# Performance work log

Hardware: AMD Instinct MI355X
Metric: run time of the kernel (lower is better)

The kernel has to match this reference:

```python
import jax, jax.numpy as jnp
import numpy as np

E, T, D_IN, D_H = 8, 2048, 2048, 5632


def setup_inputs() -> dict:
    key = jax.random.key(0)
    kx, kg, kd, ku = jax.random.split(key, 4)
    scale = 0.02  # init_std-like scaling for weights
    return {
        "x": jax.random.normal(kx, (E, T, D_IN), dtype=jnp.float32),
        "gate_proj": jax.random.normal(kg, (E, D_IN, D_H), dtype=jnp.float32) * scale,
        "down_proj": jax.random.normal(kd, (E, D_IN, D_H), dtype=jnp.float32) * scale,
        "up_proj": jax.random.normal(ku, (E, D_H, D_IN), dtype=jnp.float32) * scale,
        "tokens_per_expert": T,
    }


def reference(x, gate_proj, down_proj, up_proj, tokens_per_expert):
    # ep_size=1: dispatch/combine are identity. Grouped SwiGLU per expert.
    # x: [E, T, d_in]; gate/down: [E, d_in, d_h]; up: [E, d_h, d_in]
    g = jnp.einsum('etd,edh->eth', x, gate_proj)
    u = jnp.einsum('etd,edh->eth', x, down_proj)
    h = jax.nn.silu(g) * u  # [E, T, d_h]
    out = jnp.einsum('eth,ehd->etd', h, up_proj)  # [E, T, d_in]
    return out
```

## Files before the change

kernel.cpp:

```cpp
#include <hip/hip_runtime.h>
#include <hip/hip_bf16.h>


#define NEXP 8
#define TT   2048
#define DIN  2048
#define DH   5632
#define KP   2080

using short8 = __attribute__((ext_vector_type(8))) short;
using f32x4  = __attribute__((ext_vector_type(4))) float;

static __device__ __forceinline__ unsigned short f2bf(float f) {
    unsigned int i = __float_as_uint(f);
    return (unsigned short)((i + 0x7FFFu + ((i >> 16) & 1u)) >> 16);
}
static __device__ __forceinline__ void gld16(const void* g, void* l) {
    __builtin_amdgcn_global_load_lds(
        (const __attribute__((address_space(1))) void*)g,
        (__attribute__((address_space(3))) void*)l, 16, 0, 0);
}

__global__ __launch_bounds__(512, 2) void gemm_gu(
    const unsigned short* __restrict__ Xb,
    const unsigned short* __restrict__ Wgt,
    const unsigned short* __restrict__ Wdt,
    unsigned short* __restrict__ Hb)
{
    __shared__ __align__(16) unsigned short lds[81920];

    const int tid  = threadIdx.x;
    const int wave = tid >> 6, lane = tid & 63;
    const int l15 = lane & 15, l4 = lane >> 4;
    const int wr = wave >> 2, wc = wave & 3;

    const int bid = blockIdx.x;
    const int e   = bid & 7;
    const int cu  = bid >> 3;
    const int m0  = (cu & 7) * 256;
    const int nb  = cu >> 3;

    const unsigned short* Ae = Xb + (size_t)e * TT * KP;
    unsigned short* He = Hb + (size_t)e * TT * DH;

    const int c0 = tid, c1 = 512 + tid;
    const int cs0 = c0 ^ ((c0 >> 3) & 7), cs1 = c1 ^ ((c1 >> 3) & 7);
    const int row0 = cs0 >> 3, col0 = (cs0 & 7) * 8;
    const int row1 = cs1 >> 3, col1 = (cs1 & 7) * 8;

    int ibA[4][2], ibB[2][2];
#pragma unroll
    for (int s = 0; s < 4; ++s)
#pragma unroll
        for (int ks = 0; ks < 2; ++ks) {
            const int r = wr * 64 + s * 16 + l15;
            ibA[s][ks] = (r * 128 + ks * 64 + l4 * 16) ^ ((r & 7) << 4);
        }
#pragma unroll
    for (int s = 0; s < 2; ++s)
#pragma unroll
        for (int ks = 0; ks < 2; ++ks) {
            const int r = wc * 32 + s * 16 + l15;
            ibB[s][ks] = (r * 128 + ks * 64 + l4 * 16) ^ ((r & 7) << 4);
        }

    f32x4 acc[8][4] = {};
    short8 Aq[4][2], Gq[2][2], Dq[2][2];

    char* ldsb = (char*)lds;
    auto stageA = [&](int ro, int kk, int so) {
        gld16(Ae + (size_t)(m0 + ro + row0) * KP + (kk + col0), ldsb + so + wave * 1024);
        gld16(Ae + (size_t)(m0 + ro + row1) * KP + (kk + col1), ldsb + so + 8192 + wave * 1024);
    };
    auto stageW = [&](const unsigned short* p, int kk, int so) {
        gld16(p + (size_t)row0 * KP + (kk + col0), ldsb + so + wave * 1024);
        gld16(p + (size_t)row1 * KP + (kk + col1), ldsb + so + 8192 + wave * 1024);
    };
    auto w10 = [](int x) { return x >= 10 ? x - 10 : x; };

    const size_t NSTEP = (size_t)512 * KP;
    const unsigned short* Gc = Wgt + (size_t)e * DH * KP + (size_t)(nb * 128) * KP;
    const unsigned short* Dc = Wdt + (size_t)e * DH * KP + (size_t)(nb * 128) * KP;

    stageA(0, 0, 0 << 14);  stageW(Gc, 0, 1 << 14);  stageW(Dc, 0, 2 << 14);  stageA(128, 0, 3 << 14);
    stageA(0, 64, 4 << 14); stageW(Gc, 64, 5 << 14); stageW(Dc, 64, 6 << 14);
    asm volatile("s_waitcnt vmcnt(6)" ::: "memory");
    asm volatile("s_barrier" ::: "memory");

    const char* ldsc = (const char*)lds;
    int q = 0;
    for (int i = 0; i < 11; ++i) {
        const unsigned short* Gn = Gc + NSTEP;
        const unsigned short* Dn = Dc + NSTEP;
        for (int t = 0; t < 32; ++t) {
            const int g = (i << 5) + t;
            const int sA0 = q << 14;
            const int sG  = w10(q + 1) << 14;
            const int sD  = w10(q + 2) << 14;
            const int sA1 = w10(q + 3) << 14;
            const int stA1 = w10(q + 7) << 14;
            const int stA0 = w10(q + 8) << 14;
            const int stG  = w10(q + 9) << 14;
            const int stD  = sA0;

#pragma unroll
            for (int s = 0; s < 4; ++s) {
                Aq[s][0] = *(const short8*)(ldsc + sA0 + ibA[s][0]);
                Aq[s][1] = *(const short8*)(ldsc + sA0 + ibA[s][1]);
            }
#pragma unroll
            for (int s = 0; s < 2; ++s) {
                Gq[s][0] = *(const short8*)(ldsc + sG + ibB[s][0]);
                Gq[s][1] = *(const short8*)(ldsc + sG + ibB[s][1]);
                Dq[s][0] = *(const short8*)(ldsc + sD + ibB[s][0]);
                Dq[s][1] = *(const short8*)(ldsc + sD + ibB[s][1]);
            }
            if (i < 10 || t + 1 < 32)
                stageA(128, ((t + 1) & 31) * 64, stA1);
            asm volatile("s_waitcnt lgkmcnt(0)" ::: "memory");
            __builtin_amdgcn_sched_barrier(0);
            __builtin_amdgcn_s_setprio(1);
#pragma unroll
            for (int m = 0; m < 4; ++m)
#pragma unroll
                for (int n = 0; n < 2; ++n) {
                    acc[m][n] = __builtin_amdgcn_mfma_f32_16x16x32_bf16(Aq[m][0], Gq[n][0], acc[m][n], 0, 0, 0);
                    acc[m][n] = __builtin_amdgcn_mfma_f32_16x16x32_bf16(Aq[m][1], Gq[n][1], acc[m][n], 0, 0, 0);
                }
            __builtin_amdgcn_s_setprio(0);
            if (i < 10 || t + 2 < 32)
                stageA(0, ((t + 2) & 31) * 64, stA0);
            __builtin_amdgcn_s_setprio(1);
#pragma unroll
            for (int m = 0; m < 4; ++m)
#pragma unroll
                for (int n = 0; n < 2; ++n) {
                    acc[m][2 + n] = __builtin_amdgcn_mfma_f32_16x16x32_bf16(Aq[m][0], Dq[n][0], acc[m][2 + n], 0, 0, 0);
                    acc[m][2 + n] = __builtin_amdgcn_mfma_f32_16x16x32_bf16(Aq[m][1], Dq[n][1], acc[m][2 + n], 0, 0, 0);
                }
            __builtin_amdgcn_s_setprio(0);
#pragma unroll
            for (int s = 0; s < 4; ++s) {
                Aq[s][0] = *(const short8*)(ldsc + sA1 + ibA[s][0]);
                Aq[s][1] = *(const short8*)(ldsc + sA1 + ibA[s][1]);
            }
            if (i < 10 || t + 2 < 32)
                stageW((t + 2 < 32) ? Gc : Gn, ((t + 2) & 31) * 64, stG);
            asm volatile("s_waitcnt lgkmcnt(0)" ::: "memory");
            __builtin_amdgcn_sched_barrier(0);
            __builtin_amdgcn_s_setprio(1);
#pragma unroll
            for (int m = 0; m < 4; ++m)
#pragma unroll
                for (int n = 0; n < 2; ++n) {
                    acc[4 + m][2 + n] = __builtin_amdgcn_mfma_f32_16x16x32_bf16(Aq[m][0], Dq[n][0], acc[4 + m][2 + n], 0, 0, 0);
                    acc[4 + m][2 + n] = __builtin_amdgcn_mfma_f32_16x16x32_bf16(Aq[m][1], Dq[n][1], acc[4 + m][2 + n], 0, 0, 0);
                }
#pragma unroll
            for (int m = 0; m < 4; ++m)
#pragma unroll
                for (int n = 0; n < 2; ++n) {
                    acc[4 + m][n] = __builtin_amdgcn_mfma_f32_16x16x32_bf16(Aq[m][0], Gq[n][0], acc[4 + m][n], 0, 0, 0);
                    acc[4 + m][n] = __builtin_amdgcn_mfma_f32_16x16x32_bf16(Aq[m][1], Gq[n][1], acc[4 + m][n], 0, 0, 0);
                }
            __builtin_amdgcn_s_setprio(0);
            asm volatile("s_barrier" ::: "memory");
            if (i < 10 || t + 2 < 32)
                stageW((t + 2 < 32) ? Dc : Dn, ((t + 2) & 31) * 64, stD);
            if (g < 350)       asm volatile("s_waitcnt vmcnt(6)" ::: "memory");
            else if (g == 350) asm volatile("s_waitcnt vmcnt(0)" ::: "memory");
            asm volatile("s_barrier" ::: "memory");
            q = w10(q + 4);
        }

        const int n0i = (4 * i + nb) * 128;
#pragma unroll
        for (int fm = 0; fm < 8; ++fm) {
            const int row_b = m0 + (fm >> 2) * 128 + wr * 64 + (fm & 3) * 16 + l4 * 4;
#pragma unroll
            for (int nr = 0; nr < 2; ++nr) {
                const int col = n0i + wc * 32 + nr * 16 + l15;
#pragma unroll
                for (int j = 0; j < 4; ++j) {
                    const float gv = acc[fm][nr][j];
                    const float uv = acc[fm][2 + nr][j];
                    const float h = gv / (1.f + __expf(-gv)) * uv;
                    He[(size_t)(row_b + j) * DH + col] = f2bf(h);
                }
            }
        }
#pragma unroll
        for (int m = 0; m < 8; ++m)
#pragma unroll
            for (int n = 0; n < 4; ++n)
                acc[m][n] = (f32x4){0.f, 0.f, 0.f, 0.f};
        Gc = Gn; Dc = Dn;
    }
}

__global__ __launch_bounds__(512, 2) void gemm_out(
    const unsigned short* __restrict__ Ab,
    const unsigned short* __restrict__ Btb,
    float* __restrict__ Cf)
{
    __shared__ __align__(16) unsigned short lds[81920];

    const int tid  = threadIdx.x;
    const int wave = tid >> 6, lane = tid & 63;
    const int l15 = lane & 15, l4 = lane >> 4;
    const int wr = wave >> 2, wc = wave & 3;

    const int bid = blockIdx.x;
    const int e   = bid & 7;
    const int cu  = bid >> 3;
    const int m0  = (cu & 7) * 256;
    const int nb  = cu >> 3;

    const int N = DIN, K = DH;
    const unsigned short* Ae = Ab + (size_t)e * TT * DH;

    const int c0 = tid, c1 = 512 + tid;
    const int cs0 = c0 ^ ((c0 >> 3) & 7), cs1 = c1 ^ ((c1 >> 3) & 7);
    const int row0 = cs0 >> 3, col0 = (cs0 & 7) * 8;
    const int row1 = cs1 >> 3, col1 = (cs1 & 7) * 8;

    int ibA[4][2], ibB[2][2];
#pragma unroll
    for (int s = 0; s < 4; ++s)
#pragma unroll
        for (int ks = 0; ks < 2; ++ks) {
            const int r = wr * 64 + s * 16 + l15;
            ibA[s][ks] = (r * 128 + ks * 64 + l4 * 16) ^ ((r & 7) << 4);
        }
#pragma unroll
    for (int s = 0; s < 2; ++s)
#pragma unroll
        for (int ks = 0; ks < 2; ++ks) {
            const int r = wc * 32 + s * 16 + l15;
            ibB[s][ks] = (r * 128 + ks * 64 + l4 * 16) ^ ((r & 7) << 4);
        }

    f32x4 acc[8][4] = {};
    short8 Aq[4][2], B0q[2][2], B1q[2][2];

    char* ldsb = (char*)lds;
    auto stageA = [&](int ro, int kk, int so) {
        gld16(Ae + (size_t)(m0 + ro + row0) * K + (kk + col0), ldsb + so + wave * 1024);
        gld16(Ae + (size_t)(m0 + ro + row1) * K + (kk + col1), ldsb + so + 8192 + wave * 1024);
    };
    auto stageB = [&](const unsigned short* base, int co, int kk, int so) {
        gld16(base + (size_t)(co + row0) * K + (kk + col0), ldsb + so + wave * 1024);
        gld16(base + (size_t)(co + row1) * K + (kk + col1), ldsb + so + 8192 + wave * 1024);
    };
    auto w10 = [](int x) { return x >= 10 ? x - 10 : x; };

    const size_t NSTEP = (size_t)1024 * K;
    const unsigned short* Bc = Btb + (size_t)e * DIN * DH + (size_t)(nb * 256) * K;

    stageA(0, 0, 0 << 14); stageB(Bc, 0, 0, 1 << 14); stageB(Bc, 128, 0, 2 << 14); stageA(128, 0, 3 << 14);
    stageA(0, 64, 4 << 14); stageB(Bc, 0, 64, 5 << 14); stageB(Bc, 128, 64, 6 << 14);
    asm volatile("s_waitcnt vmcnt(6)" ::: "memory");
    asm volatile("s_barrier" ::: "memory");

    const char* ldsc = (const char*)lds;
    int q = 0;
    for (int i = 0; i < 2; ++i) {
        const unsigned short* Bn = Bc + NSTEP;
        for (int t = 0; t < 88; ++t) {
            const int g = i * 88 + t;
            const int sA0 = q << 14;
            const int sB0 = w10(q + 1) << 14;
            const int sB1 = w10(q + 2) << 14;
            const int sA1 = w10(q + 3) << 14;
            const int stA1 = w10(q + 7) << 14;
            const int stA0 = w10(q + 8) << 14;
            const int stB0 = w10(q + 9) << 14;
            const int stB1 = sA0;

#pragma unroll
            for (int s = 0; s < 4; ++s) {
                Aq[s][0] = *(const short8*)(ldsc + sA0 + ibA[s][0]);
                Aq[s][1] = *(const short8*)(ldsc + sA0 + ibA[s][1]);
            }
#pragma unroll
            for (int s = 0; s < 2; ++s) {
                B0q[s][0] = *(const short8*)(ldsc + sB0 + ibB[s][0]);
                B0q[s][1] = *(const short8*)(ldsc + sB0 + ibB[s][1]);
                B1q[s][0] = *(const short8*)(ldsc + sB1 + ibB[s][0]);
                B1q[s][1] = *(const short8*)(ldsc + sB1 + ibB[s][1]);
            }
            {
                const int tt = t + 1;
                if (i < 1 || tt < 88)
                    stageA(128, (tt >= 88 ? tt - 88 : tt) * 64, stA1);
            }
            asm volatile("s_waitcnt lgkmcnt(0)" ::: "memory");
            __builtin_amdgcn_sched_barrier(0);
            __builtin_amdgcn_s_setprio(1);
#pragma unroll
            for (int m = 0; m < 4; ++m)
#pragma unroll
                for (int n = 0; n < 2; ++n) {
                    acc[m][n] = __builtin_amdgcn_mfma_f32_16x16x32_bf16(Aq[m][0], B0q[n][0], acc[m][n], 0, 0, 0);
                    acc[m][n] = __builtin_amdgcn_mfma_f32_16x16x32_bf16(Aq[m][1], B0q[n][1], acc[m][n], 0, 0, 0);
                }
            __builtin_amdgcn_s_setprio(0);
            {
                const int tt = t + 2;
                if (i < 1 || tt < 88)
                    stageA(0, (tt >= 88 ? tt - 88 : tt) * 64, stA0);
            }
            __builtin_amdgcn_s_setprio(1);
#pragma unroll
            for (int m = 0; m < 4; ++m)
#pragma unroll
                for (int n = 0; n < 2; ++n) {
                    acc[m][2 + n] = __builtin_amdgcn_mfma_f32_16x16x32_bf16(Aq[m][0], B1q[n][0], acc[m][2 + n], 0, 0, 0);
                    acc[m][2 + n] = __builtin_amdgcn_mfma_f32_16x16x32_bf16(Aq[m][1], B1q[n][1], acc[m][2 + n], 0, 0, 0);
                }
            __builtin_amdgcn_s_setprio(0);
#pragma unroll
            for (int s = 0; s < 4; ++s) {
                Aq[s][0] = *(const short8*)(ldsc + sA1 + ibA[s][0]);
                Aq[s][1] = *(const short8*)(ldsc + sA1 + ibA[s][1]);
            }
            {
                const int tt = t + 2;
                if (i < 1 || tt < 88)
                    stageB((tt >= 88 ? Bn : Bc), 0, (tt >= 88 ? tt - 88 : tt) * 64, stB0);
            }
            asm volatile("s_waitcnt lgkmcnt(0)" ::: "memory");
            __builtin_amdgcn_sched_barrier(0);
            __builtin_amdgcn_s_setprio(1);
#pragma unroll
            for (int m = 0; m < 4; ++m)
#pragma unroll
                for (int n = 0; n < 2; ++n) {
                    acc[4 + m][2 + n] = __builtin_amdgcn_mfma_f32_16x16x32_bf16(Aq[m][0], B1q[n][0], acc[4 + m][2 + n], 0, 0, 0);
                    acc[4 + m][2 + n] = __builtin_amdgcn_mfma_f32_16x16x32_bf16(Aq[m][1], B1q[n][1], acc[4 + m][2 + n], 0, 0, 0);
                }
#pragma unroll
            for (int m = 0; m < 4; ++m)
#pragma unroll
                for (int n = 0; n < 2; ++n) {
                    acc[4 + m][n] = __builtin_amdgcn_mfma_f32_16x16x32_bf16(Aq[m][0], B0q[n][0], acc[4 + m][n], 0, 0, 0);
                    acc[4 + m][n] = __builtin_amdgcn_mfma_f32_16x16x32_bf16(Aq[m][1], B0q[n][1], acc[4 + m][n], 0, 0, 0);
                }
            __builtin_amdgcn_s_setprio(0);
            asm volatile("s_barrier" ::: "memory");
            {
                const int tt = t + 2;
                if (i < 1 || tt < 88)
                    stageB((tt >= 88 ? Bn : Bc), 128, (tt >= 88 ? tt - 88 : tt) * 64, stB1);
            }
            if (g < 174)       asm volatile("s_waitcnt vmcnt(6)" ::: "memory");
            else if (g == 174) asm volatile("s_waitcnt vmcnt(0)" ::: "memory");
            asm volatile("s_barrier" ::: "memory");
            q = w10(q + 4);
        }

        const int n0i = (4 * i + nb) * 256;
        float* Ce = Cf + (size_t)e * TT * DIN;
#pragma unroll
        for (int fm = 0; fm < 8; ++fm) {
            const int row_b = (fm >> 2) * 128 + wr * 64 + (fm & 3) * 16 + l4 * 4;
#pragma unroll
            for (int fn = 0; fn < 4; ++fn) {
                const int col = n0i + (fn >> 1) * 128 + wc * 32 + (fn & 1) * 16 + l15;
#pragma unroll
                for (int j = 0; j < 4; ++j)
                    Ce[(size_t)(m0 + row_b + j) * N + col] = acc[fm][fn][j];
            }
        }
#pragma unroll
        for (int m = 0; m < 8; ++m)
#pragma unroll
            for (int n = 0; n < 4; ++n)
                acc[m][n] = (f32x4){0.f, 0.f, 0.f, 0.f};
        Bc = Bn;
    }
}

__global__ __launch_bounds__(256) void transpose_f32_bf16(
    const float* __restrict__ in, unsigned short* __restrict__ out,
    int R, int C, int opitch, size_t ies, size_t oes)
{
    in  += (size_t)blockIdx.z * ies;
    out += (size_t)blockIdx.z * oes;
    __shared__ unsigned short t[64][65];
    const int tid = threadIdx.x;
    const int lr = tid >> 4, lc = (tid & 15) * 4;
    const int r0 = blockIdx.y * 64, c0 = blockIdx.x * 64;
#pragma unroll
    for (int i = 0; i < 4; ++i) {
        const int row = lr + i * 16;
        const float4 v = *(const float4*)(in + (size_t)(r0 + row) * C + c0 + lc);
        t[row][lc + 0] = f2bf(v.x); t[row][lc + 1] = f2bf(v.y);
        t[row][lc + 2] = f2bf(v.z); t[row][lc + 3] = f2bf(v.w);
    }
    __syncthreads();
#pragma unroll
    for (int i = 0; i < 4; ++i) {
        const int crow = lr + i * 16;
        ushort4 wv;
        wv.x = t[lc + 0][crow]; wv.y = t[lc + 1][crow];
        wv.z = t[lc + 2][crow]; wv.w = t[lc + 3][crow];
        *(ushort4*)(out + (size_t)(c0 + crow) * opitch + r0 + lc) = wv;
    }
}

__global__ __launch_bounds__(256) void conv_pad_f32_bf16(
    const float* __restrict__ in, unsigned short* __restrict__ out, int n8)
{
    int i = blockIdx.x * 256 + threadIdx.x;
    const int stride = gridDim.x * 256;
    for (; i < n8; i += stride) {
        const int row = i >> 8;
        const int col = (i & 255) * 8;
        const float4 v0 = *(const float4*)(in + (size_t)row * DIN + col);
        const float4 v1 = *(const float4*)(in + (size_t)row * DIN + col + 4);
        ushort4 a, b;
        a.x = f2bf(v0.x); a.y = f2bf(v0.y); a.z = f2bf(v0.z); a.w = f2bf(v0.w);
        b.x = f2bf(v1.x); b.y = f2bf(v1.y); b.z = f2bf(v1.z); b.w = f2bf(v1.w);
        *(ushort4*)(out + (size_t)row * KP + col) = a;
        *(ushort4*)(out + (size_t)row * KP + col + 4) = b;
    }
}

extern "C" void kernel_launch(void* const* d_in, const int* in_sizes, int n_in,
                              void* d_out, int out_size, void* d_ws, size_t ws_size,
                              hipStream_t stream)
{
    const float* x  = (const float*)d_in[0];
    const float* wg = (const float*)d_in[1];
    const float* wd = (const float*)d_in[2];
    const float* wu = (const float*)d_in[3];
    float* out = (float*)d_out;

    const size_t XSZ = (size_t)TT * KP;
    const size_t WPSZ = (size_t)DH * KP;
    const size_t WSZ = (size_t)DIN * DH;
    unsigned short* xb  = (unsigned short*)d_ws;
    unsigned short* wgt = xb  + (size_t)NEXP * XSZ;
    unsigned short* wdt = wgt + (size_t)NEXP * WPSZ;
    unsigned short* hb  = wdt + (size_t)NEXP * WPSZ;

    conv_pad_f32_bf16<<<4096, 256, 0, stream>>>(x, xb, NEXP * TT * (DIN / 8));
    transpose_f32_bf16<<<dim3(DH / 64, DIN / 64, NEXP), 256, 0, stream>>>(
        wg, wgt, DIN, DH, KP, WSZ, WPSZ);
    transpose_f32_bf16<<<dim3(DH / 64, DIN / 64, NEXP), 256, 0, stream>>>(
        wd, wdt, DIN, DH, KP, WSZ, WPSZ);
    gemm_gu<<<256, 512, 0, stream>>>(xb, wgt, wdt, hb);
    transpose_f32_bf16<<<dim3(DIN / 64, DH / 64, NEXP), 256, 0, stream>>>(
        wu, wgt, DH, DIN, DH, WSZ, WSZ);
    gemm_out<<<256, 512, 0, stream>>>(hb, wgt, out);
}
```

Before: 1.324 ms.

## Switch GEMM kernels to 32x32x16 MFMA tiles with restructured LDS fragment loads

Both GEMM kernels swap 16x16x32 bf16 MFMAs for 32x32x16 MFMAs, with 16-element accumulators per tile and new LDS fragment offsets. Larger MFMA tiles reuse each LDS fragment across more output, so fewer LDS reads are needed per FLOP. The loop is also restructured: all global-to-LDS prefetches for the next stages are issued up front, and LDS reads are interleaved with MFMAs per k-slice in place of the previous hand-split phases with setprio. This changes the overlap between compute and memory issue and may raise register pressure under the 512-thread, 2-blocks-per-CU launch bound.

```diff
diff --git a/kernel.cpp b/kernel.cpp
--- a/kernel.cpp
+++ b/kernel.cpp
@@ -9,7 +9,7 @@
 #define KP   2080
 
 using short8 = __attribute__((ext_vector_type(8))) short;
-using f32x4  = __attribute__((ext_vector_type(4))) float;
+using f32x16 = __attribute__((ext_vector_type(16))) float;
 
 static __device__ __forceinline__ unsigned short f2bf(float f) {
     unsigned int i = __float_as_uint(f);
@@ -31,7 +31,7 @@
 
     const int tid  = threadIdx.x;
     const int wave = tid >> 6, lane = tid & 63;
-    const int l15 = lane & 15, l4 = lane >> 4;
+    const int l31 = lane & 31, lh = lane >> 5;
     const int wr = wave >> 2, wc = wave & 3;
 
     const int bid = blockIdx.x;
@@ -40,41 +40,43 @@
     const int m0  = (cu & 7) * 256;
     const int nb  = cu >> 3;
 
-    const unsigned short* Ae = Xb + (size_t)e * TT * KP;
+    const unsigned short* Ae = Xb + (size_t)e * TT * KP + (size_t)m0 * KP;
+    const unsigned short* Ae128 = Ae + (size_t)128 * KP;
     unsigned short* He = Hb + (size_t)e * TT * DH;
 
     const int c0 = tid, c1 = 512 + tid;
     const int cs0 = c0 ^ ((c0 >> 3) & 7), cs1 = c1 ^ ((c1 >> 3) & 7);
     const int row0 = cs0 >> 3, col0 = (cs0 & 7) * 8;
     const int row1 = cs1 >> 3, col1 = (cs1 & 7) * 8;
-
-    int ibA[4][2], ibB[2][2];
-#pragma unroll
-    for (int s = 0; s < 4; ++s)
-#pragma unroll
-        for (int ks = 0; ks < 2; ++ks) {
-            const int r = wr * 64 + s * 16 + l15;
-            ibA[s][ks] = (r * 128 + ks * 64 + l4 * 16) ^ ((r & 7) << 4);
-        }
-#pragma unroll
-    for (int s = 0; s < 2; ++s)
-#pragma unroll
-        for (int ks = 0; ks < 2; ++ks) {
-            const int r = wc * 32 + s * 16 + l15;
-            ibB[s][ks] = (r * 128 + ks * 64 + l4 * 16) ^ ((r & 7) << 4);
-        }
-
-    f32x4 acc[8][4] = {};
-    short8 Aq[4][2], Gq[2][2], Dq[2][2];
+    const size_t loff0 = (size_t)row0 * KP + col0;
+    const size_t loff1 = (size_t)row1 * KP + col1;
+    const int wvoff = wave * 1024;
+
+    int ibA[2][4], ibB[4];
+#pragma unroll
+    for (int rg = 0; rg < 2; ++rg)
+#pragma unroll
+        for (int ks = 0; ks < 4; ++ks) {
+            const int r = wr * 64 + rg * 32 + l31;
+            ibA[rg][ks] = (r * 128 + ks * 32 + lh * 16) ^ ((r & 7) << 4);
+        }
+#pragma unroll
+    for (int ks = 0; ks < 4; ++ks) {
+        const int r = wc * 32 + l31;
+        ibB[ks] = (r * 128 + ks * 32 + lh * 16) ^ ((r & 7) << 4);
+    }
+
+    f32x16 accG[4] = {}, accU[4] = {};
 
     char* ldsb = (char*)lds;
+    const char* ldsc = (const char*)lds;
     auto stageA = [&](int ro, int kk, int so) {
-        gld16(Ae + (size_t)(m0 + ro + row0) * KP + (kk + col0), ldsb + so + wave * 1024);
-        gld16(Ae + (size_t)(m0 + ro + row1) * KP + (kk + col1), ldsb + so + 8192 + wave * 1024);
+        gld16(Ae + (size_t)ro * KP + kk + loff0, ldsb + so + wvoff);
+        gld16(Ae + (size_t)ro * KP + kk + loff1, ldsb + so + 8192 + wvoff);
     };
     auto stageW = [&](const unsigned short* p, int kk, int so) {
-        gld16(p + (size_t)row0 * KP + (kk + col0), ldsb + so + wave * 1024);
-        gld16(p + (size_t)row1 * KP + (kk + col1), ldsb + so + 8192 + wave * 1024);
+        gld16(p + kk + loff0, ldsb + so + wvoff);
+        gld16(p + kk + loff1, ldsb + so + 8192 + wvoff);
     };
     auto w10 = [](int x) { return x >= 10 ? x - 10 : x; };
 
@@ -87,7 +89,6 @@
     asm volatile("s_waitcnt vmcnt(6)" ::: "memory");
     asm volatile("s_barrier" ::: "memory");
 
-    const char* ldsc = (const char*)lds;
     int q = 0;
     for (int i = 0; i < 11; ++i) {
         const unsigned short* Gn = Gc + NSTEP;
@@ -103,70 +104,36 @@
             const int stG  = w10(q + 9) << 14;
             const int stD  = sA0;
 
-#pragma unroll
-            for (int s = 0; s < 4; ++s) {
-                Aq[s][0] = *(const short8*)(ldsc + sA0 + ibA[s][0]);
-                Aq[s][1] = *(const short8*)(ldsc + sA0 + ibA[s][1]);
-            }
-#pragma unroll
-            for (int s = 0; s < 2; ++s) {
-                Gq[s][0] = *(const short8*)(ldsc + sG + ibB[s][0]);
-                Gq[s][1] = *(const short8*)(ldsc + sG + ibB[s][1]);
-                Dq[s][0] = *(const short8*)(ldsc + sD + ibB[s][0]);
-                Dq[s][1] = *(const short8*)(ldsc + sD + ibB[s][1]);
-            }
             if (i < 10 || t + 1 < 32)
                 stageA(128, ((t + 1) & 31) * 64, stA1);
+            if (i < 10 || t + 2 < 32) {
+                stageA(0, ((t + 2) & 31) * 64, stA0);
+                stageW((t < 30) ? Gc : Gn, ((t + 2) & 31) * 64, stG);
+            }
+
+            short8 aF[4][4], gF[4], dF[4];
+#pragma unroll
+            for (int ks = 0; ks < 4; ++ks) {
+                aF[0][ks] = *(const short8*)(ldsc + sA0 + ibA[0][ks]);
+                aF[1][ks] = *(const short8*)(ldsc + sA0 + ibA[1][ks]);
+                aF[2][ks] = *(const short8*)(ldsc + sA1 + ibA[0][ks]);
+                aF[3][ks] = *(const short8*)(ldsc + sA1 + ibA[1][ks]);
+                gF[ks] = *(const short8*)(ldsc + sG + ibB[ks]);
+                dF[ks] = *(const short8*)(ldsc + sD + ibB[ks]);
+#pragma unroll
+                for (int mt = 0; mt < 4; ++mt) {
+                    accG[mt] = __builtin_amdgcn_mfma_f32_32x32x16_bf16(
+                        aF[mt][ks], gF[ks], accG[mt], 0, 0, 0);
+                    accU[mt] = __builtin_amdgcn_mfma_f32_32x32x16_bf16(
+                        aF[mt][ks], dF[ks], accU[mt], 0, 0, 0);
+                }
+            }
+
             asm volatile("s_waitcnt lgkmcnt(0)" ::: "memory");
             __builtin_amdgcn_sched_barrier(0);
-            __builtin_amdgcn_s_setprio(1);
-#pragma unroll
-            for (int m = 0; m < 4; ++m)
-#pragma unroll
-                for (int n = 0; n < 2; ++n) {
-                    acc[m][n] = __builtin_amdgcn_mfma_f32_16x16x32_bf16(Aq[m][0], Gq[n][0], acc[m][n], 0, 0, 0);
-                    acc[m][n] = __builtin_amdgcn_mfma_f32_16x16x32_bf16(Aq[m][1], Gq[n][1], acc[m][n], 0, 0, 0);
-                }
-            __builtin_amdgcn_s_setprio(0);
-            if (i < 10 || t + 2 < 32)
-                stageA(0, ((t + 2) & 31) * 64, stA0);
-            __builtin_amdgcn_s_setprio(1);
-#pragma unroll
-            for (int m = 0; m < 4; ++m)
-#pragma unroll
-                for (int n = 0; n < 2; ++n) {
-                    acc[m][2 + n] = __builtin_amdgcn_mfma_f32_16x16x32_bf16(Aq[m][0], Dq[n][0], acc[m][2 + n], 0, 0, 0);
-                    acc[m][2 + n] = __builtin_amdgcn_mfma_f32_16x16x32_bf16(Aq[m][1], Dq[n][1], acc[m][2 + n], 0, 0, 0);
-                }
-            __builtin_amdgcn_s_setprio(0);
-#pragma unroll
-            for (int s = 0; s < 4; ++s) {
-                Aq[s][0] = *(const short8*)(ldsc + sA1 + ibA[s][0]);
-                Aq[s][1] = *(const short8*)(ldsc + sA1 + ibA[s][1]);
-            }
-            if (i < 10 || t + 2 < 32)
-                stageW((t + 2 < 32) ? Gc : Gn, ((t + 2) & 31) * 64, stG);
-            asm volatile("s_waitcnt lgkmcnt(0)" ::: "memory");
-            __builtin_amdgcn_sched_barrier(0);
-            __builtin_amdgcn_s_setprio(1);
-#pragma unroll
-            for (int m = 0; m < 4; ++m)
-#pragma unroll
-                for (int n = 0; n < 2; ++n) {
-                    acc[4 + m][2 + n] = __builtin_amdgcn_mfma_f32_16x16x32_bf16(Aq[m][0], Dq[n][0], acc[4 + m][2 + n], 0, 0, 0);
-                    acc[4 + m][2 + n] = __builtin_amdgcn_mfma_f32_16x16x32_bf16(Aq[m][1], Dq[n][1], acc[4 + m][2 + n], 0, 0, 0);
-                }
-#pragma unroll
-            for (int m = 0; m < 4; ++m)
-#pragma unroll
-                for (int n = 0; n < 2; ++n) {
-                    acc[4 + m][n] = __builtin_amdgcn_mfma_f32_16x16x32_bf16(Aq[m][0], Gq[n][0], acc[4 + m][n], 0, 0, 0);
-                    acc[4 + m][n] = __builtin_amdgcn_mfma_f32_16x16x32_bf16(Aq[m][1], Gq[n][1], acc[4 + m][n], 0, 0, 0);
-                }
-            __builtin_amdgcn_s_setprio(0);
             asm volatile("s_barrier" ::: "memory");
             if (i < 10 || t + 2 < 32)
-                stageW((t + 2 < 32) ? Dc : Dn, ((t + 2) & 31) * 64, stD);
+                stageW((t < 30) ? Dc : Dn, ((t + 2) & 31) * 64, stD);
             if (g < 350)       asm volatile("s_waitcnt vmcnt(6)" ::: "memory");
             else if (g == 350) asm volatile("s_waitcnt vmcnt(0)" ::: "memory");
             asm volatile("s_barrier" ::: "memory");
@@ -174,26 +141,23 @@
         }
 
         const int n0i = (4 * i + nb) * 128;
-#pragma unroll
-        for (int fm = 0; fm < 8; ++fm) {
-            const int row_b = m0 + (fm >> 2) * 128 + wr * 64 + (fm & 3) * 16 + l4 * 4;
-#pragma unroll
-            for (int nr = 0; nr < 2; ++nr) {
-                const int col = n0i + wc * 32 + nr * 16 + l15;
-#pragma unroll
-                for (int j = 0; j < 4; ++j) {
-                    const float gv = acc[fm][nr][j];
-                    const float uv = acc[fm][2 + nr][j];
-                    const float h = gv / (1.f + __expf(-gv)) * uv;
-                    He[(size_t)(row_b + j) * DH + col] = f2bf(h);
-                }
-            }
-        }
-#pragma unroll
-        for (int m = 0; m < 8; ++m)
-#pragma unroll
-            for (int n = 0; n < 4; ++n)
-                acc[m][n] = (f32x4){0.f, 0.f, 0.f, 0.f};
+        const int col = n0i + wc * 32 + l31;
+#pragma unroll
+        for (int mt = 0; mt < 4; ++mt) {
+            const int row_b = m0 + (mt >> 1) * 128 + wr * 64 + (mt & 1) * 32 + 4 * lh;
+#pragma unroll
+            for (int j = 0; j < 16; ++j) {
+                const int row = row_b + (j & 3) + 8 * (j >> 2);
+                const float gv = accG[mt][j];
+                const float uv = accU[mt][j];
+                const float h = gv / (1.f + __expf(-gv)) * uv;
+                He[(size_t)row * DH + col] = f2bf(h);
+            }
+        }
+#pragma unroll
+        for (int mt = 0; mt < 4; ++mt)
+#pragma unroll
+            for (int j = 0; j < 16; ++j) { accG[mt][j] = 0.f; accU[mt][j] = 0.f; }
         Gc = Gn; Dc = Dn;
     }
 }
@@ -207,7 +171,7 @@
 
     const int tid  = threadIdx.x;
     const int wave = tid >> 6, lane = tid & 63;
-    const int l15 = lane & 15, l4 = lane >> 4;
+    const int l31 = lane & 31, lh = lane >> 5;
     const int wr = wave >> 2, wc = wave & 3;
 
     const int bid = blockIdx.x;
@@ -216,53 +180,52 @@
     const int m0  = (cu & 7) * 256;
     const int nb  = cu >> 3;
 
-    const int N = DIN, K = DH;
-    const unsigned short* Ae = Ab + (size_t)e * TT * DH;
+    const unsigned short* Ae = Ab + (size_t)e * TT * DH + (size_t)m0 * DH;
 
     const int c0 = tid, c1 = 512 + tid;
     const int cs0 = c0 ^ ((c0 >> 3) & 7), cs1 = c1 ^ ((c1 >> 3) & 7);
     const int row0 = cs0 >> 3, col0 = (cs0 & 7) * 8;
     const int row1 = cs1 >> 3, col1 = (cs1 & 7) * 8;
-
-    int ibA[4][2], ibB[2][2];
-#pragma unroll
-    for (int s = 0; s < 4; ++s)
-#pragma unroll
-        for (int ks = 0; ks < 2; ++ks) {
-            const int r = wr * 64 + s * 16 + l15;
-            ibA[s][ks] = (r * 128 + ks * 64 + l4 * 16) ^ ((r & 7) << 4);
-        }
-#pragma unroll
-    for (int s = 0; s < 2; ++s)
-#pragma unroll
-        for (int ks = 0; ks < 2; ++ks) {
-            const int r = wc * 32 + s * 16 + l15;
-            ibB[s][ks] = (r * 128 + ks * 64 + l4 * 16) ^ ((r & 7) << 4);
-        }
-
-    f32x4 acc[8][4] = {};
-    short8 Aq[4][2], B0q[2][2], B1q[2][2];
+    const size_t loff0 = (size_t)row0 * DH + col0;
+    const size_t loff1 = (size_t)row1 * DH + col1;
+    const int wvoff = wave * 1024;
+
+    int ibA[2][4], ibB[4];
+#pragma unroll
+    for (int rg = 0; rg < 2; ++rg)
+#pragma unroll
+        for (int ks = 0; ks < 4; ++ks) {
+            const int r = wr * 64 + rg * 32 + l31;
+            ibA[rg][ks] = (r * 128 + ks * 32 + lh * 16) ^ ((r & 7) << 4);
+        }
+#pragma unroll
+    for (int ks = 0; ks < 4; ++ks) {
+        const int r = wc * 32 + l31;
+        ibB[ks] = (r * 128 + ks * 32 + lh * 16) ^ ((r & 7) << 4);
+    }
+
+    f32x16 acc[4][2] = {};
 
     char* ldsb = (char*)lds;
+    const char* ldsc = (const char*)lds;
     auto stageA = [&](int ro, int kk, int so) {
-        gld16(Ae + (size_t)(m0 + ro + row0) * K + (kk + col0), ldsb + so + wave * 1024);
-        gld16(Ae + (size_t)(m0 + ro + row1) * K + (kk + col1), ldsb + so + 8192 + wave * 1024);
+        gld16(Ae + (size_t)ro * DH + kk + loff0, ldsb + so + wvoff);
+        gld16(Ae + (size_t)ro * DH + kk + loff1, ldsb + so + 8192 + wvoff);
     };
     auto stageB = [&](const unsigned short* base, int co, int kk, int so) {
-        gld16(base + (size_t)(co + row0) * K + (kk + col0), ldsb + so + wave * 1024);
-        gld16(base + (size_t)(co + row1) * K + (kk + col1), ldsb + so + 8192 + wave * 1024);
+        gld16(base + (size_t)co * DH + kk + loff0, ldsb + so + wvoff);
+        gld16(base + (size_t)co * DH + kk + loff1, ldsb + so + 8192 + wvoff);
     };
     auto w10 = [](int x) { return x >= 10 ? x - 10 : x; };
 
-    const size_t NSTEP = (size_t)1024 * K;
-    const unsigned short* Bc = Btb + (size_t)e * DIN * DH + (size_t)(nb * 256) * K;
+    const size_t NSTEP = (size_t)1024 * DH;
+    const unsigned short* Bc = Btb + (size_t)e * DIN * DH + (size_t)(nb * 256) * DH;
 
     stageA(0, 0, 0 << 14); stageB(Bc, 0, 0, 1 << 14); stageB(Bc, 128, 0, 2 << 14); stageA(128, 0, 3 << 14);
     stageA(0, 64, 4 << 14); stageB(Bc, 0, 64, 5 << 14); stageB(Bc, 128, 64, 6 << 14);
     asm volatile("s_waitcnt vmcnt(6)" ::: "memory");
     asm volatile("s_barrier" ::: "memory");
 
-    const char* ldsc = (const char*)lds;
     int q = 0;
     for (int i = 0; i < 2; ++i) {
         const unsigned short* Bn = Bc + NSTEP;
@@ -277,81 +240,44 @@
             const int stB0 = w10(q + 9) << 14;
             const int stB1 = sA0;
 
-#pragma unroll
-            for (int s = 0; s < 4; ++s) {
-                Aq[s][0] = *(const short8*)(ldsc + sA0 + ibA[s][0]);
-                Aq[s][1] = *(const short8*)(ldsc + sA0 + ibA[s][1]);
-            }
-#pragma unroll
-            for (int s = 0; s < 2; ++s) {
-                B0q[s][0] = *(const short8*)(ldsc + sB0 + ibB[s][0]);
-                B0q[s][1] = *(const short8*)(ldsc + sB0 + ibB[s][1]);
-                B1q[s][0] = *(const short8*)(ldsc + sB1 + ibB[s][0]);
-                B1q[s][1] = *(const short8*)(ldsc + sB1 + ibB[s][1]);
-            }
             {
-                const int tt = t + 1;
-                if (i < 1 || tt < 88)
-                    stageA(128, (tt >= 88 ? tt - 88 : tt) * 64, stA1);
-            }
+                const int t1 = t + 1;
+                if (i < 1 || t1 < 88)
+                    stageA(128, (t1 >= 88 ? t1 - 88 : t1) * 64, stA1);
+            }
+            {
+                const int t2 = t + 2;
+                if (i < 1 || t2 < 88) {
+                    stageA(0, (t2 >= 88 ? t2 - 88 : t2) * 64, stA0);
+                    stageB((t2 >= 88 ? Bn : Bc), 0, (t2 >= 88 ? t2 - 88 : t2) * 64, stB0);
+                }
+            }
+
+            short8 aF[4][4], bF[2][4];
+#pragma unroll
+            for (int ks = 0; ks < 4; ++ks) {
+                aF[0][ks] = *(const short8*)(ldsc + sA0 + ibA[0][ks]);
+                aF[1][ks] = *(const short8*)(ldsc + sA0 + ibA[1][ks]);
+                aF[2][ks] = *(const short8*)(ldsc + sA1 + ibA[0][ks]);
+                aF[3][ks] = *(const short8*)(ldsc + sA1 + ibA[1][ks]);
+                bF[0][ks] = *(const short8*)(ldsc + sB0 + ibB[ks]);
+                bF[1][ks] = *(const short8*)(ldsc + sB1 + ibB[ks]);
+#pragma unroll
+                for (int mt = 0; mt < 4; ++mt) {
+                    acc[mt][0] = __builtin_amdgcn_mfma_f32_32x32x16_bf16(
+                        aF[mt][ks], bF[0][ks], acc[mt][0], 0, 0, 0);
+                    acc[mt][1] = __builtin_amdgcn_mfma_f32_32x32x16_bf16(
+                        aF[mt][ks], bF[1][ks], acc[mt][1], 0, 0, 0);
+                }
+            }
+
             asm volatile("s_waitcnt lgkmcnt(0)" ::: "memory");
             __builtin_amdgcn_sched_barrier(0);
-            __builtin_amdgcn_s_setprio(1);
-#pragma unroll
-            for (int m = 0; m < 4; ++m)
-#pragma unroll
-                for (int n = 0; n < 2; ++n) {
-                    acc[m][n] = __builtin_amdgcn_mfma_f32_16x16x32_bf16(Aq[m][0], B0q[n][0], acc[m][n], 0, 0, 0);
-                    acc[m][n] = __builtin_amdgcn_mfma_f32_16x16x32_bf16(Aq[m][1], B0q[n][1], acc[m][n], 0, 0, 0);
-                }
-            __builtin_amdgcn_s_setprio(0);
-            {
-                const int tt = t + 2;
-                if (i < 1 || tt < 88)
-                    stageA(0, (tt >= 88 ? tt - 88 : tt) * 64, stA0);
-            }
-            __builtin_amdgcn_s_setprio(1);
-#pragma unroll
-            for (int m = 0; m < 4; ++m)
-#pragma unroll
-                for (int n = 0; n < 2; ++n) {
-                    acc[m][2 + n] = __builtin_amdgcn_mfma_f32_16x16x32_bf16(Aq[m][0], B1q[n][0], acc[m][2 + n], 0, 0, 0);
-                    acc[m][2 + n] = __builtin_amdgcn_mfma_f32_16x16x32_bf16(Aq[m][1], B1q[n][1], acc[m][2 + n], 0, 0, 0);
-                }
-            __builtin_amdgcn_s_setprio(0);
-#pragma unroll
-            for (int s = 0; s < 4; ++s) {
-                Aq[s][0] = *(const short8*)(ldsc + sA1 + ibA[s][0]);
-                Aq[s][1] = *(const short8*)(ldsc + sA1 + ibA[s][1]);
-            }
-            {
-                const int tt = t + 2;
-                if (i < 1 || tt < 88)
-                    stageB((tt >= 88 ? Bn : Bc), 0, (tt >= 88 ? tt - 88 : tt) * 64, stB0);
-            }
-            asm volatile("s_waitcnt lgkmcnt(0)" ::: "memory");
-            __builtin_amdgcn_sched_barrier(0);
-            __builtin_amdgcn_s_setprio(1);
-#pragma unroll
-            for (int m = 0; m < 4; ++m)
-#pragma unroll
-                for (int n = 0; n < 2; ++n) {
-                    acc[4 + m][2 + n] = __builtin_amdgcn_mfma_f32_16x16x32_bf16(Aq[m][0], B1q[n][0], acc[4 + m][2 + n], 0, 0, 0);
-                    acc[4 + m][2 + n] = __builtin_amdgcn_mfma_f32_16x16x32_bf16(Aq[m][1], B1q[n][1], acc[4 + m][2 + n], 0, 0, 0);
-                }
-#pragma unroll
-            for (int m = 0; m < 4; ++m)
-#pragma unroll
-                for (int n = 0; n < 2; ++n) {
-                    acc[4 + m][n] = __builtin_amdgcn_mfma_f32_16x16x32_bf16(Aq[m][0], B0q[n][0], acc[4 + m][n], 0, 0, 0);
-                    acc[4 + m][n] = __builtin_amdgcn_mfma_f32_16x16x32_bf16(Aq[m][1], B0q[n][1], acc[4 + m][n], 0, 0, 0);
-                }
-            __builtin_amdgcn_s_setprio(0);
             asm volatile("s_barrier" ::: "memory");
             {
-                const int tt = t + 2;
-                if (i < 1 || tt < 88)
-                    stageB((tt >= 88 ? Bn : Bc), 128, (tt >= 88 ? tt - 88 : tt) * 64, stB1);
+                const int t2 = t + 2;
+                if (i < 1 || t2 < 88)
+                    stageB((t2 >= 88 ? Bn : Bc), 128, (t2 >= 88 ? t2 - 88 : t2) * 64, stB1);
             }
             if (g < 174)       asm volatile("s_waitcnt vmcnt(6)" ::: "memory");
             else if (g == 174) asm volatile("s_waitcnt vmcnt(0)" ::: "memory");
@@ -362,21 +288,24 @@
         const int n0i = (4 * i + nb) * 256;
         float* Ce = Cf + (size_t)e * TT * DIN;
 #pragma unroll
-        for (int fm = 0; fm < 8; ++fm) {
-            const int row_b = (fm >> 2) * 128 + wr * 64 + (fm & 3) * 16 + l4 * 4;
-#pragma unroll
-            for (int fn = 0; fn < 4; ++fn) {
-                const int col = n0i + (fn >> 1) * 128 + wc * 32 + (fn & 1) * 16 + l15;
-#pragma unroll
-                for (int j = 0; j < 4; ++j)
-                    Ce[(size_t)(m0 + row_b + j) * N + col] = acc[fm][fn][j];
-            }
-        }
-#pragma unroll
-        for (int m = 0; m < 8; ++m)
-#pragma unroll
-            for (int n = 0; n < 4; ++n)
-                acc[m][n] = (f32x4){0.f, 0.f, 0.f, 0.f};
+        for (int mt = 0; mt < 4; ++mt) {
+            const int row_b = m0 + (mt >> 1) * 128 + wr * 64 + (mt & 1) * 32 + 4 * lh;
+#pragma unroll
+            for (int nt = 0; nt < 2; ++nt) {
+                const int col = n0i + nt * 128 + wc * 32 + l31;
+#pragma unroll
+                for (int j = 0; j < 16; ++j) {
+                    const int row = row_b + (j & 3) + 8 * (j >> 2);
+                    Ce[(size_t)row * DIN + col] = acc[mt][nt][j];
+                }
+            }
+        }
+#pragma unroll
+        for (int mt = 0; mt < 4; ++mt)
+#pragma unroll
+            for (int nt = 0; nt < 2; ++nt)
+#pragma unroll
+                for (int j = 0; j < 16; ++j) acc[mt][nt][j] = 0.f;
         Bc = Bn;
     }
 }
```

Result: slower. 1.434 ms (+8.3%).
